# Performance work log

Measured on AMD Instinct MI355X. Metric: run time of the kernel, lower is better.

## Reference

```python
import jax, jax.numpy as jnp
import numpy as np

B, D, H, L, T = 4096, 256, 512, 2, 45


def _lstm_cell(x, h, c, W_ih, W_hh, b_ih, b_hh):
    # PyTorch LSTM gate order: i, f, g, o
    gates = x @ W_ih + h @ W_hh + b_ih + b_hh  # [B, 4H]
    i, f, g, o = jnp.split(gates, 4, axis=-1)
    i = jax.nn.sigmoid(i)
    f = jax.nn.sigmoid(f)
    g = jnp.tanh(g)
    o = jax.nn.sigmoid(o)
    c_new = f * c + i * g
    h_new = o * jnp.tanh(c_new)
    return h_new, c_new


def setup_inputs() -> dict:
    key = jax.random.key(0)
    ks = jax.random.split(key, 32)
    s = 0.02
    inp = {
        "encoder_feat": jax.random.normal(ks[0], (B, D), jnp.float32),
        "context": jax.random.normal(ks[1], (B, D), jnp.float32),
        "initial_intent": jax.random.uniform(ks[2], (B, 1), jnp.float32),
        # hidden/cell init linears: d_model -> H*L (stored [in, out])
        "Wh_init": jax.random.normal(ks[3], (D, H * L), jnp.float32) * s,
        "bh_init": jnp.zeros((H * L,), jnp.float32),
        "Wc_init": jax.random.normal(ks[4], (D, H * L), jnp.float32) * s,
        "bc_init": jnp.zeros((H * L,), jnp.float32),
        # LSTM layer 0: input size 1 + d_model
        "W_ih0": jax.random.normal(ks[5], (1 + D, 4 * H), jnp.float32) * s,
        "W_hh0": jax.random.normal(ks[6], (H, 4 * H), jnp.float32) * s,
        "b_ih0": jnp.zeros((4 * H,), jnp.float32),
        "b_hh0": jnp.zeros((4 * H,), jnp.float32),
        # LSTM layer 1: input size H
        "W_ih1": jax.random.normal(ks[7], (H, 4 * H), jnp.float32) * s,
        "W_hh1": jax.random.normal(ks[8], (H, 4 * H), jnp.float32) * s,
        "b_ih1": jnp.zeros((4 * H,), jnp.float32),
        "b_hh1": jnp.zeros((4 * H,), jnp.float32),
        # output_proj: H -> 32 -> 1
        "Wo1": jax.random.normal(ks[9], (H, 32), jnp.float32) * s,
        "bo1": jnp.zeros((32,), jnp.float32),
        "Wo2": jax.random.normal(ks[10], (32, 1), jnp.float32) * s,
        "bo2": jnp.zeros((1,), jnp.float32),
        # global_intent_head: H -> 32 -> 1
        "Wg1": jax.random.normal(ks[11], (H, 32), jnp.float32) * s,
        "bg1": jnp.zeros((32,), jnp.float32),
        "Wg2": jax.random.normal(ks[12], (32, 1), jnp.float32) * s,
        "bg2": jnp.zeros((1,), jnp.float32),
    }
    return inp


def reference(encoder_feat, context, initial_intent,
              Wh_init, bh_init, Wc_init, bc_init,
              W_ih0, W_hh0, b_ih0, b_hh0,
              W_ih1, W_hh1, b_ih1, b_hh1,
              Wo1, bo1, Wo2, bo2, Wg1, bg1, Wg2, bg2):
    # init hidden/cell: [B, L*H] -> [B, L, H]; layer-major slices
    h_init = (encoder_feat @ Wh_init + bh_init).reshape(B, L, H)
    c_init = (encoder_feat @ Wc_init + bc_init).reshape(B, L, H)
    h0, h1 = h_init[:, 0], h_init[:, 1]
    c0, c1 = c_init[:, 0], c_init[:, 1]

    def step(carry, _):
        h0, c0, h1, c1, intent = carry
        x = jnp.concatenate([intent, context], axis=-1)  # [B, 1+D]
        h0n, c0n = _lstm_cell(x, h0, c0, W_ih0, W_hh0, b_ih0, b_hh0)
        h1n, c1n = _lstm_cell(h0n, h1, c1, W_ih1, W_hh1, b_ih1, b_hh1)
        logit = jax.nn.relu(h1n @ Wo1 + bo1) @ Wo2 + bo2  # [B, 1]
        intent_new = jax.nn.sigmoid(logit)
        return (h0n, c0n, h1n, c1n, intent_new), intent_new

    carry0 = (h0, c0, h1, c1, initial_intent)
    (h0, c0, h1, c1, _), ys = jax.lax.scan(step, carry0, None, length=T)
    step_intents = jnp.transpose(ys, (1, 0, 2))  # [B, T, 1]
    global_logit = jax.nn.relu(h1 @ Wg1 + bg1) @ Wg2 + bg2
    global_intent = jax.nn.sigmoid(global_logit)  # [B, 1]
    return step_intents, global_intent
```

## Files before the change

kernel.cpp:

```cpp
#include <hip/hip_runtime.h>
#include <hip/hip_bf16.h>

#define Bsz 4096
#define Dsz 256
#define Hsz 512
#define Tsz 45

typedef __attribute__((ext_vector_type(8))) short short8;
typedef __attribute__((ext_vector_type(4))) float f32x4;
using bf16 = __hip_bfloat16;

__device__ __forceinline__ float sigf(float x)   { return 1.0f / (1.0f + __expf(-x)); }
__device__ __forceinline__ float tanhft(float x) { return 1.0f - 2.0f / (__expf(2.0f * x) + 1.0f); }

__device__ __forceinline__ void gload16(const void* g, void* l) {
    __builtin_amdgcn_global_load_lds((const __attribute__((address_space(1))) void*)g,
                                     (__attribute__((address_space(3))) void*)l, 16, 0, 0);
}

__global__ void k_conv(const float* __restrict__ ef,   const float* __restrict__ ctx,
                       const float* __restrict__ Whi,  const float* __restrict__ Wci,
                       const float* __restrict__ Wih0, const float* __restrict__ Whh0,
                       const float* __restrict__ Wih1, const float* __restrict__ Whh1,
                       const float* __restrict__ Wo1,  const float* __restrict__ Wg1,
                       bf16* __restrict__ efb,  bf16* __restrict__ ctxb,
                       bf16* __restrict__ Wit,  bf16* __restrict__ Wt0,
                       bf16* __restrict__ Wt1,  bf16* __restrict__ Wo1t,
                       bf16* __restrict__ Wg1t)
{
    size_t tid = (size_t)blockIdx.x * blockDim.x + threadIdx.x;
    size_t gsz = (size_t)gridDim.x * blockDim.x;
    for (size_t i = tid; i < (size_t)Bsz * Dsz; i += gsz) {
        efb[i]  = __float2bfloat16(ef[i]);
        ctxb[i] = __float2bfloat16(ctx[i]);
    }
    for (size_t i = tid; i < 2048ull * 512; i += gsz) {
        size_t n = i >> 9, k = i & 511;
        Wt0[i] = __float2bfloat16(Whh0[k * 2048 + n]);
    }
    for (size_t i = tid; i < 2048ull * 1024; i += gsz) {
        size_t n = i >> 10, k = i & 1023;
        Wt1[i] = __float2bfloat16(k < 512 ? Wih1[k * 2048 + n] : Whh1[(k - 512) * 2048 + n]);
    }
    for (size_t i = tid; i < 32ull * 512; i += gsz) {
        size_t c = i >> 9, k = i & 511;
        Wo1t[i] = __float2bfloat16(Wo1[k * 32 + c]);
        Wg1t[i] = __float2bfloat16(Wg1[k * 32 + c]);
    }
    for (size_t i = tid; i < 4096ull * 256; i += gsz) {
        size_t n = i >> 8, k = i & 255;
        float v = (n < 1024) ? Whi[k * 1024 + n]
                : (n < 2048) ? Wci[k * 1024 + (n - 1024)]
                             : Wih0[(1 + k) * 2048 + (n - 2048)];
        Wit[i] = __float2bfloat16(v);
    }
}

__global__ void __launch_bounds__(256)
k_init(const bf16* __restrict__ efb, const bf16* __restrict__ ctxb,
       const bf16* __restrict__ Wit,
       const float* __restrict__ bh,  const float* __restrict__ bc,
       const float* __restrict__ bi0, const float* __restrict__ bh0,
       bf16* __restrict__ h0, bf16* __restrict__ h1,
       float* __restrict__ c0, float* __restrict__ c1,
       bf16* __restrict__ ctxg)
{
    const int t = threadIdx.x, lane = t & 63, w = t >> 6;
    const int wr = w >> 1, wc = w & 1;
    const int lq = lane >> 4, ln = lane & 15;
    const int m0 = blockIdx.x * 128, n0 = blockIdx.y * 64;
    const bf16* A = (n0 < 2048) ? efb : ctxb;

    f32x4 zero = {0.f, 0.f, 0.f, 0.f};
    f32x4 acc[4][2];
#pragma unroll
    for (int r = 0; r < 4; ++r)
#pragma unroll
        for (int c = 0; c < 2; ++c) acc[r][c] = zero;

    for (int k0 = 0; k0 < 256; k0 += 32) {
        short8 af[4];
#pragma unroll
        for (int r = 0; r < 4; ++r)
            af[r] = *(const short8*)(A + (size_t)(m0 + wr * 64 + r * 16 + ln) * 256 + k0 + lq * 8);
#pragma unroll
        for (int c = 0; c < 2; ++c) {
            short8 bv = *(const short8*)(Wit + (size_t)(n0 + wc * 32 + c * 16 + ln) * 256 + k0 + lq * 8);
#pragma unroll
            for (int r = 0; r < 4; ++r)
                acc[r][c] = __builtin_amdgcn_mfma_f32_16x16x32_bf16(af[r], bv, acc[r][c], 0, 0, 0);
        }
    }
#pragma unroll
    for (int r = 0; r < 4; ++r)
#pragma unroll
        for (int c = 0; c < 2; ++c)
#pragma unroll
            for (int e = 0; e < 4; ++e) {
                int b = m0 + wr * 64 + r * 16 + lq * 4 + e;
                int n = n0 + wc * 32 + c * 16 + ln;
                float v = acc[r][c][e];
                if (n < 1024) {
                    v += bh[n];
                    if (n < 512) h0[(size_t)b * 512 + n]       = __float2bfloat16(v);
                    else         h1[(size_t)b * 512 + n - 512] = __float2bfloat16(v);
                } else if (n < 2048) {
                    int m = n - 1024; v += bc[m];
                    if (m < 512) c0[(size_t)b * 512 + m]       = v;
                    else         c1[(size_t)b * 512 + m - 512] = v;
                } else {
                    int j = n - 2048;
                    ctxg[(size_t)b * 2048 + j] = __float2bfloat16(v + bi0[j] + bh0[j]);
                }
            }
}

template <int L0>
__global__ void __launch_bounds__(256)
k_gates(const bf16* __restrict__ hA, const bf16* __restrict__ hB,
        const bf16* __restrict__ Wt,
        const bf16* __restrict__ ctxg, const float* __restrict__ intent,
        const float* __restrict__ w0row,
        const float* __restrict__ b1, const float* __restrict__ b2,
        float* __restrict__ cbuf, bf16* __restrict__ hout)
{
    constexpr int KW = L0 ? 512 : 1024;
    __shared__ __align__(16) bf16 As[128 * 32];
    __shared__ __align__(16) bf16 Bs[4 * 32 * 32];
    const int t = threadIdx.x;
    const int lane = t & 63, w = t >> 6;
    const int wr = w >> 1, wc = w & 1;
    const int lq = lane >> 4, ln = lane & 15;
    const int m0 = blockIdx.x * 128, j0 = blockIdx.y * 32;

    f32x4 zero = {0.f, 0.f, 0.f, 0.f};
    f32x4 acc[4][4];
#pragma unroll
    for (int g = 0; g < 4; ++g)
#pragma unroll
        for (int r = 0; r < 4; ++r) acc[g][r] = zero;

    for (int k0 = 0; k0 < KW; k0 += 32) {
        __syncthreads();
#pragma unroll
        for (int i = 0; i < 2; ++i) {
            int chunk = i * 256 + t;
            int row = chunk >> 2, kc = chunk & 3;
            int kk = k0 + (kc ^ ((row >> 2) & 3)) * 8;
            const bf16* src;
            if (L0) src = hA + (size_t)(m0 + row) * Hsz + kk;
            else    src = (k0 < 512) ? hA + (size_t)(m0 + row) * Hsz + kk
                                     : hB + (size_t)(m0 + row) * Hsz + (kk - 512);
            gload16(src, (char*)As + (size_t)(i * 256 + w * 64) * 16);
        }
#pragma unroll
        for (int i = 0; i < 2; ++i) {
            int chunk = i * 256 + t;
            int g = chunk >> 7, rem = chunk & 127;
            int n = rem >> 2, kc = rem & 3;
            int kk = k0 + (kc ^ ((n >> 2) & 3)) * 8;
            const bf16* src = Wt + (size_t)(g * 512 + j0 + n) * KW + kk;
            gload16(src, (char*)Bs + (size_t)(i * 256 + w * 64) * 16);
        }
        __syncthreads();

        short8 af[4];
#pragma unroll
        for (int r = 0; r < 4; ++r) {
            int row = wr * 64 + r * 16 + ln;
            int c = lq ^ ((row >> 2) & 3);
            af[r] = *(const short8*)(As + row * 32 + c * 8);
        }
#pragma unroll
        for (int g = 0; g < 4; ++g) {
            int n = wc * 16 + ln;
            int c = lq ^ ((n >> 2) & 3);
            short8 bv = *(const short8*)(Bs + (g * 32 + n) * 32 + c * 8);
#pragma unroll
            for (int r = 0; r < 4; ++r)
                acc[g][r] = __builtin_amdgcn_mfma_f32_16x16x32_bf16(af[r], bv, acc[g][r], 0, 0, 0);
        }
    }

    const int jl = j0 + wc * 16 + ln;
    float addc[4];
#pragma unroll
    for (int g = 0; g < 4; ++g)
        addc[g] = L0 ? w0row[g * 512 + jl] : (b1[g * 512 + jl] + b2[g * 512 + jl]);

#pragma unroll
    for (int r = 0; r < 4; ++r)
#pragma unroll
        for (int e = 0; e < 4; ++e) {
            int b = m0 + wr * 64 + r * 16 + lq * 4 + e;
            float pre[4];
#pragma unroll
            for (int g = 0; g < 4; ++g) pre[g] = acc[g][r][e];
            if (L0) {
                float it = intent[b];
#pragma unroll
                for (int g = 0; g < 4; ++g)
                    pre[g] += __bfloat162float(ctxg[(size_t)b * 2048 + g * 512 + jl]) + it * addc[g];
            } else {
#pragma unroll
                for (int g = 0; g < 4; ++g) pre[g] += addc[g];
            }
            float ig = sigf(pre[0]), fg = sigf(pre[1]);
            float gg = tanhft(pre[2]), og = sigf(pre[3]);
            size_t idx = (size_t)b * Hsz + jl;
            float cn = fg * cbuf[idx] + ig * gg;
            cbuf[idx] = cn;
            hout[idx] = __float2bfloat16(og * tanhft(cn));
        }
}

__global__ void __launch_bounds__(256)
k_intent(const bf16* __restrict__ h, const bf16* __restrict__ W1t,
         const float* __restrict__ bias1, const float* __restrict__ W2,
         const float* __restrict__ bias2,
         float* __restrict__ outp, int ostride, float* __restrict__ iws)
{
    const int t = threadIdx.x, lane = t & 63, w = t >> 6;
    const int wr = w >> 1, wc = w & 1;
    const int lq = lane >> 4, ln = lane & 15;
    const int m0 = blockIdx.x * 128;
    __shared__ float part[128][2];

    f32x4 zero = {0.f, 0.f, 0.f, 0.f};
    f32x4 acc[4];
#pragma unroll
    for (int r = 0; r < 4; ++r) acc[r] = zero;

    for (int k0 = 0; k0 < 512; k0 += 32) {
        short8 bv = *(const short8*)(W1t + (size_t)(wc * 16 + ln) * 512 + k0 + lq * 8);
#pragma unroll
        for (int r = 0; r < 4; ++r) {
            short8 av = *(const short8*)(h + (size_t)(m0 + wr * 64 + r * 16 + ln) * 512 + k0 + lq * 8);
            acc[r] = __builtin_amdgcn_mfma_f32_16x16x32_bf16(av, bv, acc[r], 0, 0, 0);
        }
    }
    int col = wc * 16 + ln;
    float b1v = bias1[col], w2v = W2[col];
#pragma unroll
    for (int r = 0; r < 4; ++r)
#pragma unroll
        for (int e = 0; e < 4; ++e) {
            float v = fmaxf(acc[r][e] + b1v, 0.f) * w2v;
            v += __shfl_xor(v, 1);
            v += __shfl_xor(v, 2);
            v += __shfl_xor(v, 4);
            v += __shfl_xor(v, 8);
            if (ln == 0) part[wr * 64 + r * 16 + lq * 4 + e][wc] = v;
        }
    __syncthreads();
    if (t < 128) {
        int b = m0 + t;
        float p = sigf(part[t][0] + part[t][1] + bias2[0]);
        outp[(size_t)b * ostride] = p;
        if (iws) iws[b] = p;
    }
}

extern "C" void kernel_launch(void* const* d_in, const int* in_sizes, int n_in,
                              void* d_out, int out_size, void* d_ws, size_t ws_size,
                              hipStream_t stream)
{
    const float* ef   = (const float*)d_in[0];
    const float* ctx  = (const float*)d_in[1];
    const float* ii   = (const float*)d_in[2];
    const float* Whi  = (const float*)d_in[3];
    const float* bh   = (const float*)d_in[4];
    const float* Wci  = (const float*)d_in[5];
    const float* bc   = (const float*)d_in[6];
    const float* Wih0 = (const float*)d_in[7];
    const float* Whh0 = (const float*)d_in[8];
    const float* bi0  = (const float*)d_in[9];
    const float* bh0  = (const float*)d_in[10];
    const float* Wih1 = (const float*)d_in[11];
    const float* Whh1 = (const float*)d_in[12];
    const float* bi1  = (const float*)d_in[13];
    const float* bh1  = (const float*)d_in[14];
    const float* Wo1  = (const float*)d_in[15];
    const float* bo1  = (const float*)d_in[16];
    const float* Wo2  = (const float*)d_in[17];
    const float* bo2  = (const float*)d_in[18];
    const float* Wg1  = (const float*)d_in[19];
    const float* bg1  = (const float*)d_in[20];
    const float* Wg2  = (const float*)d_in[21];
    const float* bg2  = (const float*)d_in[22];
    float* out = (float*)d_out;

    char* ws = (char*)d_ws;
    size_t off = 0;
    auto take = [&](size_t bytes) -> char* {
        char* p = ws + off;
        off += (bytes + 255) & ~(size_t)255;
        return p;
    };
    bf16* Wt0    = (bf16*)take(2048ull * 512 * 2);
    bf16* Wt1    = (bf16*)take(2048ull * 1024 * 2);
    bf16* Wo1t   = (bf16*)take(32ull * 512 * 2);
    bf16* Wg1t   = (bf16*)take(32ull * 512 * 2);
    bf16* Wit    = (bf16*)take(4096ull * 256 * 2);
    bf16* efb    = (bf16*)take((size_t)Bsz * Dsz * 2);
    bf16* ctxb   = (bf16*)take((size_t)Bsz * Dsz * 2);
    bf16* h0b[2] = {(bf16*)take((size_t)Bsz * Hsz * 2), (bf16*)take((size_t)Bsz * Hsz * 2)};
    bf16* h1b[2] = {(bf16*)take((size_t)Bsz * Hsz * 2), (bf16*)take((size_t)Bsz * Hsz * 2)};
    float* c0    = (float*)take((size_t)Bsz * Hsz * 4);
    float* c1    = (float*)take((size_t)Bsz * Hsz * 4);
    bf16* ctxg   = (bf16*)take((size_t)Bsz * 2048 * 2);
    float* iws   = (float*)take((size_t)Bsz * 4);
    (void)ws_size; (void)in_sizes; (void)n_in; (void)out_size;

    k_conv<<<2048, 256, 0, stream>>>(ef, ctx, Whi, Wci, Wih0, Whh0, Wih1, Whh1, Wo1, Wg1,
                                     efb, ctxb, Wit, Wt0, Wt1, Wo1t, Wg1t);
    k_init<<<dim3(32, 64), 256, 0, stream>>>(efb, ctxb, Wit, bh, bc, bi0, bh0,
                                             h0b[0], h1b[0], c0, c1, ctxg);
    for (int s = 0; s < Tsz; ++s) {
        int p = s & 1;
        const float* it = (s == 0) ? ii : iws;
        k_gates<1><<<dim3(32, 16), 256, 0, stream>>>(h0b[p], nullptr, Wt0, ctxg, it, Wih0,
                                                     nullptr, nullptr, c0, h0b[1 - p]);
        k_gates<0><<<dim3(32, 16), 256, 0, stream>>>(h0b[1 - p], h1b[p], Wt1, nullptr, nullptr,
                                                     nullptr, bi1, bh1, c1, h1b[1 - p]);
        k_intent<<<32, 256, 0, stream>>>(h1b[1 - p], Wo1t, bo1, Wo2, bo2, out + s, Tsz, iws);
    }
    k_intent<<<32, 256, 0, stream>>>(h1b[1], Wg1t, bg1, Wg2, bg2, out + (size_t)Bsz * Tsz, 1, nullptr);
}
```

Baseline: 2.831 ms.

## Fuse whole LSTM time loop into one persistent kernel with FP8 weights

Replaces the 135 per-step launches (two gate kernels plus an intent head per timestep) with a single persistent kernel. Each block owns 16 batch rows, keeps h in LDS and c, context gates and biases in registers across all 45 steps, and computes both layers and the intent head in place. Weights and hidden states are converted to FP8 and pre-packed into an MFMA-friendly layout so the fp8 MFMA can be used, halving the weight bytes streamed each step. This removes launch overhead and the global round-trips of h and c, but it re-reads the full weight set from L2/HBM in every block each step and lowers numerical precision to FP8.

```diff
diff --git a/kernel.cpp b/kernel.cpp
--- a/kernel.cpp
+++ b/kernel.cpp
@@ -8,14 +8,16 @@
 
 typedef __attribute__((ext_vector_type(8))) short short8;
 typedef __attribute__((ext_vector_type(4))) float f32x4;
+typedef __attribute__((ext_vector_type(4))) unsigned short us4;
 using bf16 = __hip_bfloat16;
+using u8 = unsigned char;
 
 __device__ __forceinline__ float sigf(float x)   { return 1.0f / (1.0f + __expf(-x)); }
 __device__ __forceinline__ float tanhft(float x) { return 1.0f - 2.0f / (__expf(2.0f * x) + 1.0f); }
-
-__device__ __forceinline__ void gload16(const void* g, void* l) {
-    __builtin_amdgcn_global_load_lds((const __attribute__((address_space(1))) void*)g,
-                                     (__attribute__((address_space(3))) void*)l, 16, 0, 0);
+__device__ __forceinline__ float b2f(unsigned short u) { return __uint_as_float((unsigned)u << 16); }
+__device__ __forceinline__ u8 f2fp8(float v) {
+    int p = __builtin_amdgcn_cvt_pk_fp8_f32(v, v, 0, false);
+    return (u8)(p & 0xff);
 }
 
 __global__ void k_conv(const float* __restrict__ ef,   const float* __restrict__ ctx,
@@ -24,9 +26,9 @@
                        const float* __restrict__ Wih1, const float* __restrict__ Whh1,
                        const float* __restrict__ Wo1,  const float* __restrict__ Wg1,
                        bf16* __restrict__ efb,  bf16* __restrict__ ctxb,
-                       bf16* __restrict__ Wit,  bf16* __restrict__ Wt0,
-                       bf16* __restrict__ Wt1,  bf16* __restrict__ Wo1t,
-                       bf16* __restrict__ Wg1t)
+                       bf16* __restrict__ Wit,  u8* __restrict__ W0p,
+                       u8* __restrict__ W1p,  u8* __restrict__ Wo1p,
+                       u8* __restrict__ Wg1p)
 {
     size_t tid = (size_t)blockIdx.x * blockDim.x + threadIdx.x;
     size_t gsz = (size_t)gridDim.x * blockDim.x;
@@ -34,18 +36,38 @@
         efb[i]  = __float2bfloat16(ef[i]);
         ctxb[i] = __float2bfloat16(ctx[i]);
     }
-    for (size_t i = tid; i < 2048ull * 512; i += gsz) {
-        size_t n = i >> 9, k = i & 511;
-        Wt0[i] = __float2bfloat16(Whh0[k * 2048 + n]);
-    }
-    for (size_t i = tid; i < 2048ull * 1024; i += gsz) {
-        size_t n = i >> 10, k = i & 1023;
-        Wt1[i] = __float2bfloat16(k < 512 ? Wih1[k * 2048 + n] : Whh1[(k - 512) * 2048 + n]);
-    }
-    for (size_t i = tid; i < 32ull * 512; i += gsz) {
-        size_t c = i >> 9, k = i & 511;
-        Wo1t[i] = __float2bfloat16(Wo1[k * 32 + c]);
-        Wg1t[i] = __float2bfloat16(Wg1[k * 32 + c]);
+    for (size_t i = tid; i < 2048ull * 512 / 4; i += gsz) {
+        int n = i >> 7, k = (i & 127) * 4;
+        int lo = __builtin_amdgcn_cvt_pk_fp8_f32(Whh0[(size_t)(k+0)*2048+n], Whh0[(size_t)(k+1)*2048+n], 0, false);
+        int pk = __builtin_amdgcn_cvt_pk_fp8_f32(Whh0[(size_t)(k+2)*2048+n], Whh0[(size_t)(k+3)*2048+n], lo, true);
+        size_t dst = ((size_t)(n >> 4) * 16 + (k >> 5)) * 512 + ((k >> 3) & 3) * 128 + (n & 15) * 8 + (k & 4);
+        *(int*)(W0p + dst) = pk;
+    }
+    for (size_t i = tid; i < 2048ull * 1024 / 4; i += gsz) {
+        int n = i >> 8, k = (i & 255) * 4;
+        float f0, f1, f2, f3;
+        if (k < 512) {
+            f0 = Wih1[(size_t)(k+0)*2048+n]; f1 = Wih1[(size_t)(k+1)*2048+n];
+            f2 = Wih1[(size_t)(k+2)*2048+n]; f3 = Wih1[(size_t)(k+3)*2048+n];
+        } else {
+            int kk = k - 512;
+            f0 = Whh1[(size_t)(kk+0)*2048+n]; f1 = Whh1[(size_t)(kk+1)*2048+n];
+            f2 = Whh1[(size_t)(kk+2)*2048+n]; f3 = Whh1[(size_t)(kk+3)*2048+n];
+        }
+        int lo = __builtin_amdgcn_cvt_pk_fp8_f32(f0, f1, 0, false);
+        int pk = __builtin_amdgcn_cvt_pk_fp8_f32(f2, f3, lo, true);
+        size_t dst = ((size_t)(n >> 4) * 32 + (k >> 5)) * 512 + ((k >> 3) & 3) * 128 + (n & 15) * 8 + (k & 4);
+        *(int*)(W1p + dst) = pk;
+    }
+    for (size_t i = tid; i < 32ull * 512 / 4; i += gsz) {
+        int n = i >> 7, k = (i & 127) * 4;
+        size_t dst = ((size_t)(n >> 4) * 16 + (k >> 5)) * 512 + ((k >> 3) & 3) * 128 + (n & 15) * 8 + (k & 4);
+        int lo = __builtin_amdgcn_cvt_pk_fp8_f32(Wo1[(size_t)(k+0)*32+n], Wo1[(size_t)(k+1)*32+n], 0, false);
+        int pk = __builtin_amdgcn_cvt_pk_fp8_f32(Wo1[(size_t)(k+2)*32+n], Wo1[(size_t)(k+3)*32+n], lo, true);
+        *(int*)(Wo1p + dst) = pk;
+        lo = __builtin_amdgcn_cvt_pk_fp8_f32(Wg1[(size_t)(k+0)*32+n], Wg1[(size_t)(k+1)*32+n], 0, false);
+        pk = __builtin_amdgcn_cvt_pk_fp8_f32(Wg1[(size_t)(k+2)*32+n], Wg1[(size_t)(k+3)*32+n], lo, true);
+        *(int*)(Wg1p + dst) = pk;
     }
     for (size_t i = tid; i < 4096ull * 256; i += gsz) {
         size_t n = i >> 8, k = i & 255;
@@ -61,7 +83,7 @@
        const bf16* __restrict__ Wit,
        const float* __restrict__ bh,  const float* __restrict__ bc,
        const float* __restrict__ bi0, const float* __restrict__ bh0,
-       bf16* __restrict__ h0, bf16* __restrict__ h1,
+       u8* __restrict__ h0, u8* __restrict__ h1,
        float* __restrict__ c0, float* __restrict__ c1,
        bf16* __restrict__ ctxg)
 {
@@ -102,163 +124,196 @@
                 float v = acc[r][c][e];
                 if (n < 1024) {
                     v += bh[n];
-                    if (n < 512) h0[(size_t)b * 512 + n]       = __float2bfloat16(v);
-                    else         h1[(size_t)b * 512 + n - 512] = __float2bfloat16(v);
+                    if (n < 512) h0[(size_t)b * 512 + n]       = f2fp8(v);
+                    else         h1[(size_t)b * 512 + n - 512] = f2fp8(v);
                 } else if (n < 2048) {
                     int m = n - 1024; v += bc[m];
                     if (m < 512) c0[(size_t)b * 512 + m]       = v;
                     else         c1[(size_t)b * 512 + m - 512] = v;
                 } else {
                     int j = n - 2048;
-                    ctxg[(size_t)b * 2048 + j] = __float2bfloat16(v + bi0[j] + bh0[j]);
+                    ctxg[(size_t)b * 2048 + (j & 511) * 4 + (j >> 9)] =
+                        __float2bfloat16(v + bi0[j] + bh0[j]);
                 }
             }
 }
 
-template <int L0>
-__global__ void __launch_bounds__(256)
-k_gates(const bf16* __restrict__ hA, const bf16* __restrict__ hB,
-        const bf16* __restrict__ Wt,
-        const bf16* __restrict__ ctxg, const float* __restrict__ intent,
-        const float* __restrict__ w0row,
-        const float* __restrict__ b1, const float* __restrict__ b2,
-        float* __restrict__ cbuf, bf16* __restrict__ hout)
+__device__ __forceinline__ long aread8(const u8* buf, int ln, int lq, int kt) {
+    return *(const long*)(buf + ln * 512 + ((((kt << 2) + lq) ^ (ln & 7)) << 3));
+}
+
+__global__ void __launch_bounds__(512, 2)
+k_loop(const u8* __restrict__ h0i, const u8* __restrict__ h1i,
+       const u8* __restrict__ W0p, const u8* __restrict__ W1p,
+       const u8* __restrict__ Wo1p, const u8* __restrict__ Wg1p,
+       const bf16* __restrict__ ctxg, const float* __restrict__ ii,
+       const float* __restrict__ w0row,
+       const float* __restrict__ bi1, const float* __restrict__ bh1,
+       const float* __restrict__ bo1, const float* __restrict__ Wo2,
+       const float* __restrict__ bo2,
+       const float* __restrict__ bg1, const float* __restrict__ Wg2,
+       const float* __restrict__ bg2,
+       const float* __restrict__ c0g, const float* __restrict__ c1g,
+       float* __restrict__ out)
 {
-    constexpr int KW = L0 ? 512 : 1024;
-    __shared__ __align__(16) bf16 As[128 * 32];
-    __shared__ __align__(16) bf16 Bs[4 * 32 * 32];
-    const int t = threadIdx.x;
-    const int lane = t & 63, w = t >> 6;
-    const int wr = w >> 1, wc = w & 1;
-    const int lq = lane >> 4, ln = lane & 15;
-    const int m0 = blockIdx.x * 128, j0 = blockIdx.y * 32;
-
+    __shared__ u8 h0L[2][16 * 512];
+    __shared__ u8 h1L[2][16 * 512];
+    __shared__ float sit[16];
+    __shared__ float spart[16][2];
+
+    const int t = threadIdx.x, lane = t & 63, w = t >> 6;
+    const int ln = lane & 15, lq = lane >> 4;
+    const int m0 = blockIdx.x * 16;
     f32x4 zero = {0.f, 0.f, 0.f, 0.f};
-    f32x4 acc[4][4];
-#pragma unroll
-    for (int g = 0; g < 4; ++g)
-#pragma unroll
-        for (int r = 0; r < 4; ++r) acc[g][r] = zero;
-
-    for (int k0 = 0; k0 < KW; k0 += 32) {
+
+#pragma unroll
+    for (int i = 0; i < 2; ++i) {
+        int cid = i * 512 + t;
+        int row = cid >> 6, c = cid & 63;
+        long v0 = *(const long*)(h0i + (size_t)(m0 + row) * 512 + c * 8);
+        long v1 = *(const long*)(h1i + (size_t)(m0 + row) * 512 + c * 8);
+        int pc = row * 512 + ((c ^ (row & 7)) << 3);
+        *(long*)(&h0L[0][pc]) = v0;
+        *(long*)(&h1L[0][pc]) = v1;
+    }
+    float cr0[4][4], cr1[4][4], a0r[4][4], a1r[4][4];
+    us4 xg[4][4];
+#pragma unroll
+    for (int jc = 0; jc < 4; ++jc) {
+        int jl = jc * 128 + w * 16 + ln;
+#pragma unroll
+        for (int e = 0; e < 4; ++e) {
+            int b = m0 + lq * 4 + e;
+            cr0[jc][e] = c0g[(size_t)b * 512 + jl];
+            cr1[jc][e] = c1g[(size_t)b * 512 + jl];
+            xg[jc][e]  = *(const us4*)((const unsigned short*)ctxg + (size_t)b * 2048 + jl * 4);
+        }
+#pragma unroll
+        for (int g = 0; g < 4; ++g) {
+            a0r[jc][g] = w0row[g * 512 + jl];
+            a1r[jc][g] = bi1[g * 512 + jl] + bh1[g * 512 + jl];
+        }
+    }
+    __syncthreads();
+
+    auto head2 = [&](const u8* hbuf, const u8* Wp, const float* b1,
+                     const float* W2, float b2s, bool tosit,
+                     float* dst, int stride, int scol) {
+        if (w < 2) {
+            f32x4 acc = zero;
+            const u8* bp = Wp + ((size_t)w * 16) * 512 + lane * 8;
+#pragma unroll
+            for (int kt = 0; kt < 16; ++kt) {
+                long a = aread8(hbuf, ln, lq, kt);
+                long b = *(const long*)(bp + kt * 512);
+                acc = __builtin_amdgcn_mfma_f32_16x16x32_fp8_fp8(a, b, acc, 0, 0, 0);
+            }
+            int col = w * 16 + ln;
+            float b1v = b1[col], w2v = W2[col];
+#pragma unroll
+            for (int e = 0; e < 4; ++e) {
+                float v = fmaxf(acc[e] + b1v, 0.f) * w2v;
+                v += __shfl_xor(v, 1);
+                v += __shfl_xor(v, 2);
+                v += __shfl_xor(v, 4);
+                v += __shfl_xor(v, 8);
+                if (ln == 0) spart[lq * 4 + e][w] = v;
+            }
+        }
         __syncthreads();
-#pragma unroll
-        for (int i = 0; i < 2; ++i) {
-            int chunk = i * 256 + t;
-            int row = chunk >> 2, kc = chunk & 3;
-            int kk = k0 + (kc ^ ((row >> 2) & 3)) * 8;
-            const bf16* src;
-            if (L0) src = hA + (size_t)(m0 + row) * Hsz + kk;
-            else    src = (k0 < 512) ? hA + (size_t)(m0 + row) * Hsz + kk
-                                     : hB + (size_t)(m0 + row) * Hsz + (kk - 512);
-            gload16(src, (char*)As + (size_t)(i * 256 + w * 64) * 16);
-        }
-#pragma unroll
-        for (int i = 0; i < 2; ++i) {
-            int chunk = i * 256 + t;
-            int g = chunk >> 7, rem = chunk & 127;
-            int n = rem >> 2, kc = rem & 3;
-            int kk = k0 + (kc ^ ((n >> 2) & 3)) * 8;
-            const bf16* src = Wt + (size_t)(g * 512 + j0 + n) * KW + kk;
-            gload16(src, (char*)Bs + (size_t)(i * 256 + w * 64) * 16);
+        if (t < 16) {
+            float pv = sigf(spart[t][0] + spart[t][1] + b2s);
+            if (tosit) sit[t] = pv;
+            if (dst) dst[(size_t)(m0 + t) * stride + scol] = pv;
         }
         __syncthreads();
-
-        short8 af[4];
-#pragma unroll
-        for (int r = 0; r < 4; ++r) {
-            int row = wr * 64 + r * 16 + ln;
-            int c = lq ^ ((row >> 2) & 3);
-            af[r] = *(const short8*)(As + row * 32 + c * 8);
-        }
-#pragma unroll
-        for (int g = 0; g < 4; ++g) {
-            int n = wc * 16 + ln;
-            int c = lq ^ ((n >> 2) & 3);
-            short8 bv = *(const short8*)(Bs + (g * 32 + n) * 32 + c * 8);
-#pragma unroll
-            for (int r = 0; r < 4; ++r)
-                acc[g][r] = __builtin_amdgcn_mfma_f32_16x16x32_bf16(af[r], bv, acc[g][r], 0, 0, 0);
-        }
-    }
-
-    const int jl = j0 + wc * 16 + ln;
-    float addc[4];
-#pragma unroll
-    for (int g = 0; g < 4; ++g)
-        addc[g] = L0 ? w0row[g * 512 + jl] : (b1[g * 512 + jl] + b2[g * 512 + jl]);
-
-#pragma unroll
-    for (int r = 0; r < 4; ++r)
-#pragma unroll
-        for (int e = 0; e < 4; ++e) {
-            int b = m0 + wr * 64 + r * 16 + lq * 4 + e;
-            float pre[4];
-#pragma unroll
-            for (int g = 0; g < 4; ++g) pre[g] = acc[g][r][e];
-            if (L0) {
-                float it = intent[b];
+    };
+
+    for (int s = 0; s < Tsz; ++s) {
+        const int p = s & 1;
+        const u8* h0c = h0L[p];
+        u8*       h0n = h0L[1 - p];
+        const u8* h1c = h1L[p];
+        u8*       h1n = h1L[1 - p];
+
+        if (s == 0) {
+            if (t < 16) sit[t] = ii[m0 + t];
+            __syncthreads();
+        } else {
+            head2(h1c, Wo1p, bo1, Wo2, bo2[0], true, out, Tsz, s - 1);
+        }
+        float sreg[4];
+#pragma unroll
+        for (int e = 0; e < 4; ++e) sreg[e] = sit[lq * 4 + e];
+
+#pragma unroll 1
+        for (int jc = 0; jc < 4; ++jc) {
+            const int jl = jc * 128 + w * 16 + ln;
+            f32x4 acc[4];
+#pragma unroll
+            for (int g = 0; g < 4; ++g) acc[g] = zero;
+            const u8* bp = W0p + (((size_t)jc * 8 + w) * 16) * 512 + lane * 8;
+#pragma unroll 4
+            for (int kt = 0; kt < 16; ++kt) {
+                long a = aread8(h0c, ln, lq, kt);
+#pragma unroll
+                for (int g = 0; g < 4; ++g) {
+                    long b = *(const long*)(bp + (size_t)g * 262144 + kt * 512);
+                    acc[g] = __builtin_amdgcn_mfma_f32_16x16x32_fp8_fp8(a, b, acc[g], 0, 0, 0);
+                }
+            }
+#pragma unroll
+            for (int e = 0; e < 4; ++e) {
+                float pre[4];
 #pragma unroll
                 for (int g = 0; g < 4; ++g)
-                    pre[g] += __bfloat162float(ctxg[(size_t)b * 2048 + g * 512 + jl]) + it * addc[g];
-            } else {
-#pragma unroll
-                for (int g = 0; g < 4; ++g) pre[g] += addc[g];
-            }
-            float ig = sigf(pre[0]), fg = sigf(pre[1]);
-            float gg = tanhft(pre[2]), og = sigf(pre[3]);
-            size_t idx = (size_t)b * Hsz + jl;
-            float cn = fg * cbuf[idx] + ig * gg;
-            cbuf[idx] = cn;
-            hout[idx] = __float2bfloat16(og * tanhft(cn));
-        }
-}
-
-__global__ void __launch_bounds__(256)
-k_intent(const bf16* __restrict__ h, const bf16* __restrict__ W1t,
-         const float* __restrict__ bias1, const float* __restrict__ W2,
-         const float* __restrict__ bias2,
-         float* __restrict__ outp, int ostride, float* __restrict__ iws)
-{
-    const int t = threadIdx.x, lane = t & 63, w = t >> 6;
-    const int wr = w >> 1, wc = w & 1;
-    const int lq = lane >> 4, ln = lane & 15;
-    const int m0 = blockIdx.x * 128;
-    __shared__ float part[128][2];
-
-    f32x4 zero = {0.f, 0.f, 0.f, 0.f};
-    f32x4 acc[4];
-#pragma unroll
-    for (int r = 0; r < 4; ++r) acc[r] = zero;
-
-    for (int k0 = 0; k0 < 512; k0 += 32) {
-        short8 bv = *(const short8*)(W1t + (size_t)(wc * 16 + ln) * 512 + k0 + lq * 8);
-#pragma unroll
-        for (int r = 0; r < 4; ++r) {
-            short8 av = *(const short8*)(h + (size_t)(m0 + wr * 64 + r * 16 + ln) * 512 + k0 + lq * 8);
-            acc[r] = __builtin_amdgcn_mfma_f32_16x16x32_bf16(av, bv, acc[r], 0, 0, 0);
-        }
-    }
-    int col = wc * 16 + ln;
-    float b1v = bias1[col], w2v = W2[col];
-#pragma unroll
-    for (int r = 0; r < 4; ++r)
-#pragma unroll
-        for (int e = 0; e < 4; ++e) {
-            float v = fmaxf(acc[r][e] + b1v, 0.f) * w2v;
-            v += __shfl_xor(v, 1);
-            v += __shfl_xor(v, 2);
-            v += __shfl_xor(v, 4);
-            v += __shfl_xor(v, 8);
-            if (ln == 0) part[wr * 64 + r * 16 + lq * 4 + e][wc] = v;
-        }
-    __syncthreads();
-    if (t < 128) {
-        int b = m0 + t;
-        float p = sigf(part[t][0] + part[t][1] + bias2[0]);
-        outp[(size_t)b * ostride] = p;
-        if (iws) iws[b] = p;
-    }
+                    pre[g] = acc[g][e] + b2f(xg[jc][e][g]) + sreg[e] * a0r[jc][g];
+                float ig = sigf(pre[0]), fg = sigf(pre[1]);
+                float gg = tanhft(pre[2]), og = sigf(pre[3]);
+                float cn = fg * cr0[jc][e] + ig * gg;
+                cr0[jc][e] = cn;
+                int row = lq * 4 + e;
+                h0n[row * 512 + (((jl >> 3) ^ (row & 7)) << 3) + (jl & 7)] =
+                    f2fp8(og * tanhft(cn));
+            }
+        }
+        __syncthreads();
+
+#pragma unroll 1
+        for (int jc = 0; jc < 4; ++jc) {
+            const int jl = jc * 128 + w * 16 + ln;
+            f32x4 acc[4];
+#pragma unroll
+            for (int g = 0; g < 4; ++g) acc[g] = zero;
+            const u8* bp = W1p + (((size_t)jc * 8 + w) * 32) * 512 + lane * 8;
+#pragma unroll 4
+            for (int kt = 0; kt < 32; ++kt) {
+                long a = (kt < 16) ? aread8(h0n, ln, lq, kt) : aread8(h1c, ln, lq, kt - 16);
+#pragma unroll
+                for (int g = 0; g < 4; ++g) {
+                    long b = *(const long*)(bp + (size_t)g * 524288 + kt * 512);
+                    acc[g] = __builtin_amdgcn_mfma_f32_16x16x32_fp8_fp8(a, b, acc[g], 0, 0, 0);
+                }
+            }
+#pragma unroll
+            for (int e = 0; e < 4; ++e) {
+                float pre[4];
+#pragma unroll
+                for (int g = 0; g < 4; ++g) pre[g] = acc[g][e] + a1r[jc][g];
+                float ig = sigf(pre[0]), fg = sigf(pre[1]);
+                float gg = tanhft(pre[2]), og = sigf(pre[3]);
+                float cn = fg * cr1[jc][e] + ig * gg;
+                cr1[jc][e] = cn;
+                int row = lq * 4 + e;
+                h1n[row * 512 + (((jl >> 3) ^ (row & 7)) << 3) + (jl & 7)] =
+                    f2fp8(og * tanhft(cn));
+            }
+        }
+        __syncthreads();
+    }
+
+    head2(h1L[1], Wo1p, bo1, Wo2, bo2[0], false, out, Tsz, 44);
+    head2(h1L[1], Wg1p, bg1, Wg2, bg2[0], false, out + (size_t)Bsz * Tsz, 1, 0);
 }
 
 extern "C" void kernel_launch(void* const* d_in, const int* in_sizes, int n_in,
@@ -293,37 +348,30 @@
     char* ws = (char*)d_ws;
     size_t off = 0;
     auto take = [&](size_t bytes) -> char* {
-        char* p = ws + off;
+        char* pp = ws + off;
         off += (bytes + 255) & ~(size_t)255;
-        return p;
+        return pp;
     };
-    bf16* Wt0    = (bf16*)take(2048ull * 512 * 2);
-    bf16* Wt1    = (bf16*)take(2048ull * 1024 * 2);
-    bf16* Wo1t   = (bf16*)take(32ull * 512 * 2);
-    bf16* Wg1t   = (bf16*)take(32ull * 512 * 2);
+    u8*  W0p     = (u8*)take(2048ull * 512);
+    u8*  W1p     = (u8*)take(2048ull * 1024);
+    u8*  Wo1p    = (u8*)take(32ull * 512);
+    u8*  Wg1p    = (u8*)take(32ull * 512);
     bf16* Wit    = (bf16*)take(4096ull * 256 * 2);
     bf16* efb    = (bf16*)take((size_t)Bsz * Dsz * 2);
     bf16* ctxb   = (bf16*)take((size_t)Bsz * Dsz * 2);
-    bf16* h0b[2] = {(bf16*)take((size_t)Bsz * Hsz * 2), (bf16*)take((size_t)Bsz * Hsz * 2)};
-    bf16* h1b[2] = {(bf16*)take((size_t)Bsz * Hsz * 2), (bf16*)take((size_t)Bsz * Hsz * 2)};
+    u8*  h0x     = (u8*)take((size_t)Bsz * Hsz);
+    u8*  h1x     = (u8*)take((size_t)Bsz * Hsz);
     float* c0    = (float*)take((size_t)Bsz * Hsz * 4);
     float* c1    = (float*)take((size_t)Bsz * Hsz * 4);
     bf16* ctxg   = (bf16*)take((size_t)Bsz * 2048 * 2);
-    float* iws   = (float*)take((size_t)Bsz * 4);
     (void)ws_size; (void)in_sizes; (void)n_in; (void)out_size;
 
     k_conv<<<2048, 256, 0, stream>>>(ef, ctx, Whi, Wci, Wih0, Whh0, Wih1, Whh1, Wo1, Wg1,
-                                     efb, ctxb, Wit, Wt0, Wt1, Wo1t, Wg1t);
+                                     efb, ctxb, Wit, W0p, W1p, Wo1p, Wg1p);
     k_init<<<dim3(32, 64), 256, 0, stream>>>(efb, ctxb, Wit, bh, bc, bi0, bh0,
-                                             h0b[0], h1b[0], c0, c1, ctxg);
-    for (int s = 0; s < Tsz; ++s) {
-        int p = s & 1;
-        const float* it = (s == 0) ? ii : iws;
-        k_gates<1><<<dim3(32, 16), 256, 0, stream>>>(h0b[p], nullptr, Wt0, ctxg, it, Wih0,
-                                                     nullptr, nullptr, c0, h0b[1 - p]);
-        k_gates<0><<<dim3(32, 16), 256, 0, stream>>>(h0b[1 - p], h1b[p], Wt1, nullptr, nullptr,
-                                                     nullptr, bi1, bh1, c1, h1b[1 - p]);
-        k_intent<<<32, 256, 0, stream>>>(h1b[1 - p], Wo1t, bo1, Wo2, bo2, out + s, Tsz, iws);
-    }
-    k_intent<<<32, 256, 0, stream>>>(h1b[1], Wg1t, bg1, Wg2, bg2, out + (size_t)Bsz * Tsz, 1, nullptr);
-}
+                                             h0x, h1x, c0, c1, ctxg);
+    k_loop<<<256, 512, 0, stream>>>(h0x, h1x, W0p, W1p, Wo1p, Wg1p,
+                                    ctxg, ii, Wih0, bi1, bh1,
+                                    bo1, Wo2, bo2, bg1, Wg2, bg2,
+                                    c0, c1, out);
+}
```

Measured after the change: 4.727 ms. 1.67x slower.
